# Kernel tuning notes

Hardware: AMD Instinct MI355X
Metric: run time of the kernel (lower is better)

## Reference

```python
import jax, jax.numpy as jnp
import numpy as np

N_HEAD = 16
SCALE = True
NEG = 10000.0


def setup_inputs() -> dict:
    key = jax.random.key(0)
    ks = jax.random.split(key, 5)
    B, S, D = 4, 1024, 1024
    x = jax.random.normal(ks[0], (B, S, D), dtype=jnp.float32)
    # GPT-2 Conv1D weights: W has shape [in, out], init ~N(0, 0.02)
    w_attn = jax.random.normal(ks[1], (D, 3 * D), dtype=jnp.float32) * 0.02
    b_attn = jnp.zeros((3 * D,), dtype=jnp.float32)
    w_proj = jax.random.normal(ks[2], (D, D), dtype=jnp.float32) * 0.02
    b_proj = jnp.zeros((D,), dtype=jnp.float32)
    return {"x": x, "w_attn": w_attn, "b_attn": b_attn,
            "w_proj": w_proj, "b_proj": b_proj}


def reference(x, w_attn, b_attn, w_proj, b_proj):
    B, S, D = x.shape
    H = N_HEAD
    hd = D // H
    # c_attn: Conv1D == x @ W + b
    qkv = jnp.einsum('bsd,de->bse', x, w_attn) + b_attn
    q, k, v = jnp.split(qkv, 3, axis=-1)
    # split heads -> [B, H, S, hd]
    q = q.reshape(B, S, H, hd).transpose(0, 2, 1, 3)
    k = k.reshape(B, S, H, hd).transpose(0, 2, 1, 3)
    v = v.reshape(B, S, H, hd).transpose(0, 2, 1, 3)
    # scores [B, H, S, S]
    w = jnp.einsum('bhqd,bhkd->bhqk', q, k)
    if SCALE:
        w = w / jnp.sqrt(jnp.float32(hd))
    # multiplicative causal mask: w*b - 10000*(1-b)
    bmask = jnp.tril(jnp.ones((S, S), dtype=w.dtype))[None, None]
    w = w * bmask - NEG * (1.0 - bmask)
    w = jax.nn.softmax(w, axis=-1)
    # attn_pdrop = 0 -> dropout is identity
    a = jnp.einsum('bhqk,bhkd->bhqd', w, v)
    # merge heads
    a = a.transpose(0, 2, 1, 3).reshape(B, S, D)
    # c_proj; resid_pdrop = 0
    out = jnp.einsum('bsd,de->bse', a, w_proj) + b_proj
    return out
```

## Files before the change

kernel.cpp:

```cpp
#include <hip/hip_runtime.h>
#include <hip/hip_bf16.h>


typedef __bf16 bf16x8 __attribute__((ext_vector_type(8)));
typedef float f32x4 __attribute__((ext_vector_type(4)));

__device__ __forceinline__ void load_lds16(const void* g, void* l) {
  __builtin_amdgcn_global_load_lds(
      (const __attribute__((address_space(1))) void*)g,
      (__attribute__((address_space(3))) void*)l, 16, 0, 0);
}

__global__ __launch_bounds__(256) void f32_to_bf16(
    const float* __restrict__ in, __bf16* __restrict__ out, int n) {
  int i = (blockIdx.x * 256 + threadIdx.x) * 4;
  if (i + 3 < n) {
    float4 v = *(const float4*)(in + i);
    out[i + 0] = (__bf16)v.x;
    out[i + 1] = (__bf16)v.y;
    out[i + 2] = (__bf16)v.z;
    out[i + 3] = (__bf16)v.w;
  }
}

__global__ __launch_bounds__(256) void transpose_f32_bf16(
    const float* __restrict__ W, __bf16* __restrict__ WT, int K, int N) {
  __shared__ __bf16 tile[32][33];
  int n0 = blockIdx.x * 32, k0 = blockIdx.y * 32;
  int tx = threadIdx.x, ty = threadIdx.y;
#pragma unroll
  for (int j = 0; j < 32; j += 8)
    tile[ty + j][tx] = (__bf16)W[(size_t)(k0 + ty + j) * N + n0 + tx];
  __syncthreads();
#pragma unroll
  for (int j = 0; j < 32; j += 8)
    WT[(size_t)(n0 + ty + j) * K + k0 + tx] = tile[tx][ty + j];
}

__global__ __launch_bounds__(256) void pack_kv(
    const __bf16* __restrict__ qkv, __bf16* __restrict__ Kp,
    __bf16* __restrict__ VT) {
  const int tid = threadIdx.x;
  const int lane = tid & 63, wave = tid >> 6;
  const int bh = blockIdx.x >> 4;
  const int kb = (blockIdx.x & 15) * 64;
  const int b = bh >> 4, h = bh & 15;

  const __bf16* srcv =
      qkv + ((size_t)b * 1024 + kb + lane) * 3072 + 2048 + h * 64 + wave * 16;
  bf16x8 v0 = *(const bf16x8*)srcv;
  bf16x8 v1 = *(const bf16x8*)(srcv + 8);
  __bf16* dstv = VT + ((size_t)bh * 64 + wave * 16) * 1024 + kb + lane;
#pragma unroll
  for (int i = 0; i < 8; ++i) {
    dstv[(size_t)i * 1024] = v0[i];
    dstv[(size_t)(i + 8) * 1024] = v1[i];
  }

#pragma unroll
  for (int p = 0; p < 2; ++p) {
    const int idx = p * 256 + tid;
    const int key = kb + (idx >> 3);
    const int c = (idx & 7) * 8;
    *(bf16x8*)(Kp + (size_t)bh * 65536 + (size_t)key * 64 + c) =
        *(const bf16x8*)(qkv + ((size_t)b * 1024 + key) * 3072 + 1024 + h * 64 + c);
  }
}

template <typename OutT>
__global__ __launch_bounds__(256) void gemm_bt_bias(
    const __bf16* __restrict__ A, const __bf16* __restrict__ BT,
    const float* __restrict__ bias, OutT* __restrict__ C, int M, int N, int K) {
  __shared__ __bf16 sA[128 * 32];
  __shared__ __bf16 sB[128 * 32];

  const int tid = threadIdx.x;
  const int lane = tid & 63;
  const int wave = tid >> 6;
  const int waveM = wave >> 1, waveN = wave & 1;
  const int quad = lane >> 4;
  const int l16 = lane & 15;
  const int rowBase = blockIdx.y * 128;
  const int colBase = blockIdx.x * 128;

  const int rIn = lane >> 2;
  const int sIn = lane & 3;
  const int gc = sIn ^ (rIn & 3) ^ ((rIn >> 2) & 3);
  const int readSlot = quad ^ (l16 & 3) ^ ((l16 >> 2) & 3);

  f32x4 acc[4][4] = {};

  for (int k0 = 0; k0 < K; k0 += 32) {
    __syncthreads();
#pragma unroll
    for (int j = 0; j < 2; ++j) {
      const int rb = wave * 32 + j * 16;
      load_lds16(&A[(size_t)(rowBase + rb + rIn) * K + k0 + gc * 8], &sA[rb * 32]);
      load_lds16(&BT[(size_t)(colBase + rb + rIn) * K + k0 + gc * 8], &sB[rb * 32]);
    }
    __syncthreads();

    bf16x8 af[4], bfr[4];
#pragma unroll
    for (int mt = 0; mt < 4; ++mt)
      af[mt] = *(const bf16x8*)(&sA[(waveM * 64 + mt * 16 + l16) * 32 + readSlot * 8]);
#pragma unroll
    for (int nt = 0; nt < 4; ++nt)
      bfr[nt] = *(const bf16x8*)(&sB[(waveN * 64 + nt * 16 + l16) * 32 + readSlot * 8]);
#pragma unroll
    for (int mt = 0; mt < 4; ++mt)
#pragma unroll
      for (int nt = 0; nt < 4; ++nt)
        acc[mt][nt] = __builtin_amdgcn_mfma_f32_16x16x32_bf16(
            af[mt], bfr[nt], acc[mt][nt], 0, 0, 0);
  }

#pragma unroll
  for (int mt = 0; mt < 4; ++mt) {
    int row = rowBase + waveM * 64 + mt * 16 + quad * 4;
#pragma unroll
    for (int nt = 0; nt < 4; ++nt) {
      int col = colBase + waveN * 64 + nt * 16 + l16;
      float bv = bias[col];
#pragma unroll
      for (int r = 0; r < 4; ++r)
        C[(size_t)(row + r) * N + col] = (OutT)(acc[mt][nt][r] + bv);
    }
  }
}

__global__ __launch_bounds__(256) void attn_mfma(
    const __bf16* __restrict__ qkv, const __bf16* __restrict__ Kp,
    const __bf16* __restrict__ VT, __bf16* __restrict__ Aout) {
  __shared__ __bf16 sK[128 * 64];
  __shared__ __bf16 sV[64 * 128];
  __shared__ __bf16 sP[4 * 16 * 128];

  const int tid = threadIdx.x;
  const int lane = tid & 63;
  const int wave = tid >> 6;
  const int quad = lane >> 4;
  const int l16 = lane & 15;
  const int swq = l16 & 7;

  const int bh = blockIdx.x >> 3;
  const int pr = blockIdx.x & 7;
  const int b = bh >> 4, h = bh & 15;
  const int qbA = pr * 64, qbB = (15 - pr) * 64;
  const int ktA_max = pr >> 1, ktB_max = (15 - pr) >> 1;

  const size_t rowS = 3072;
  const __bf16* Qb = qkv + (size_t)b * 1024 * rowS + h * 64;
  const __bf16* Kb = Kp + (size_t)bh * 65536;
  const __bf16* VTb = VT + (size_t)bh * 64 * 1024;

  bf16x8 qA0A, qA1A, qA0B, qA1B;
  {
    const __bf16* qr = Qb + (size_t)(qbA + wave * 16 + l16) * rowS + quad * 8;
    qA0A = *(const bf16x8*)qr;
    qA1A = *(const bf16x8*)(qr + 32);
    qr = Qb + (size_t)(qbB + wave * 16 + l16) * rowS + quad * 8;
    qA0B = *(const bf16x8*)qr;
    qA1B = *(const bf16x8*)(qr + 32);
  }

  f32x4 OA[4] = {}, OB[4] = {};
  float psA[4] = {0.f, 0.f, 0.f, 0.f}, psB[4] = {0.f, 0.f, 0.f, 0.f};
  __bf16* pw = sP + wave * 2048;

  for (int kt = 0; kt <= ktB_max; ++kt) {
    const int kb = kt * 128;
    __syncthreads();

#pragma unroll
    for (int i = 0; i < 4; ++i) {
      const int rb = wave * 32 + i * 8;
      load_lds16(Kb + (size_t)(kb + rb + (lane >> 3)) * 64 +
                     (((lane & 7) ^ ((lane >> 3) & 7)) << 3),
                 &sK[rb * 64]);
    }
#pragma unroll
    for (int i = 0; i < 4; ++i) {
      const int db = wave * 16 + i * 4;
      const int d = db + (lane >> 4);
      load_lds16(VTb + (size_t)d * 1024 + kb + (((lane & 15) ^ (d & 7)) << 3),
                 &sV[db * 128]);
    }
    __syncthreads();

    {
      float sc[8][4];
#pragma unroll
      for (int n = 0; n < 8; ++n) {
        const int key = n * 16 + l16;
        bf16x8 kB0 = *(const bf16x8*)(&sK[key * 64 + ((quad ^ swq) << 3)]);
        bf16x8 kB1 = *(const bf16x8*)(&sK[key * 64 + (((quad + 4) ^ swq) << 3)]);
        f32x4 c = {};
        c = __builtin_amdgcn_mfma_f32_16x16x32_bf16(qA0B, kB0, c, 0, 0, 0);
        c = __builtin_amdgcn_mfma_f32_16x16x32_bf16(qA1B, kB1, c, 0, 0, 0);
#pragma unroll
        for (int r = 0; r < 4; ++r) sc[n][r] = c[r] * 0.125f;
      }
      if (kt == ktB_max) {
#pragma unroll
        for (int n = 0; n < 8; ++n) {
          const int kg = kb + n * 16 + l16;
#pragma unroll
          for (int r = 0; r < 4; ++r)
            if (kg > qbB + wave * 16 + quad * 4 + r) sc[n][r] = -1.0e30f;
        }
      }
#pragma unroll
      for (int n = 0; n < 8; ++n)
#pragma unroll
        for (int r = 0; r < 4; ++r) {
          float p = __expf(fminf(sc[n][r], 60.0f));
          sc[n][r] = p;
          psB[r] += p;
        }
      {
        const int kb8 = l16 >> 3, lo = l16 & 7;
#pragma unroll
        for (int n = 0; n < 8; ++n) {
          const int chunk = n * 2 + kb8;
#pragma unroll
          for (int r = 0; r < 4; ++r) {
            const int q = quad * 4 + r;
            pw[q * 128 + ((chunk ^ (q & 7)) << 3) + lo] = (__bf16)sc[n][r];
          }
        }
      }
#pragma unroll
      for (int cc = 0; cc < 4; ++cc) {
        bf16x8 pA = *(const bf16x8*)(&pw[l16 * 128 + (((cc * 4 + quad) ^ swq) << 3)]);
#pragma unroll
        for (int nt = 0; nt < 4; ++nt) {
          bf16x8 vB = *(const bf16x8*)(&sV[(nt * 16 + l16) * 128 +
                                           (((cc * 4 + quad) ^ swq) << 3)]);
          OB[nt] = __builtin_amdgcn_mfma_f32_16x16x32_bf16(pA, vB, OB[nt], 0, 0, 0);
        }
      }
    }

    if (kt <= ktA_max) {
      float sc[8][4];
#pragma unroll
      for (int n = 0; n < 8; ++n) {
        const int key = n * 16 + l16;
        bf16x8 kB0 = *(const bf16x8*)(&sK[key * 64 + ((quad ^ swq) << 3)]);
        bf16x8 kB1 = *(const bf16x8*)(&sK[key * 64 + (((quad + 4) ^ swq) << 3)]);
        f32x4 c = {};
        c = __builtin_amdgcn_mfma_f32_16x16x32_bf16(qA0A, kB0, c, 0, 0, 0);
        c = __builtin_amdgcn_mfma_f32_16x16x32_bf16(qA1A, kB1, c, 0, 0, 0);
#pragma unroll
        for (int r = 0; r < 4; ++r) sc[n][r] = c[r] * 0.125f;
      }
      if (kt == ktA_max) {
#pragma unroll
        for (int n = 0; n < 8; ++n) {
          const int kg = kb + n * 16 + l16;
#pragma unroll
          for (int r = 0; r < 4; ++r)
            if (kg > qbA + wave * 16 + quad * 4 + r) sc[n][r] = -1.0e30f;
        }
      }
#pragma unroll
      for (int n = 0; n < 8; ++n)
#pragma unroll
        for (int r = 0; r < 4; ++r) {
          float p = __expf(fminf(sc[n][r], 60.0f));
          sc[n][r] = p;
          psA[r] += p;
        }
      {
        const int kb8 = l16 >> 3, lo = l16 & 7;
#pragma unroll
        for (int n = 0; n < 8; ++n) {
          const int chunk = n * 2 + kb8;
#pragma unroll
          for (int r = 0; r < 4; ++r) {
            const int q = quad * 4 + r;
            pw[q * 128 + ((chunk ^ (q & 7)) << 3) + lo] = (__bf16)sc[n][r];
          }
        }
      }
#pragma unroll
      for (int cc = 0; cc < 4; ++cc) {
        bf16x8 pA = *(const bf16x8*)(&pw[l16 * 128 + (((cc * 4 + quad) ^ swq) << 3)]);
#pragma unroll
        for (int nt = 0; nt < 4; ++nt) {
          bf16x8 vB = *(const bf16x8*)(&sV[(nt * 16 + l16) * 128 +
                                           (((cc * 4 + quad) ^ swq) << 3)]);
          OA[nt] = __builtin_amdgcn_mfma_f32_16x16x32_bf16(pA, vB, OA[nt], 0, 0, 0);
        }
      }
    }
  }

  float invA[4], invB[4];
#pragma unroll
  for (int r = 0; r < 4; ++r) {
    float pa = psA[r], pb = psB[r];
    pa += __shfl_xor(pa, 1); pb += __shfl_xor(pb, 1);
    pa += __shfl_xor(pa, 2); pb += __shfl_xor(pb, 2);
    pa += __shfl_xor(pa, 4); pb += __shfl_xor(pb, 4);
    pa += __shfl_xor(pa, 8); pb += __shfl_xor(pb, 8);
    invA[r] = 1.0f / pa;
    invB[r] = 1.0f / pb;
  }
#pragma unroll
  for (int nt = 0; nt < 4; ++nt) {
#pragma unroll
    for (int r = 0; r < 4; ++r) {
      const int qA = qbA + wave * 16 + quad * 4 + r;
      const int qB = qbB + wave * 16 + quad * 4 + r;
      Aout[((size_t)b * 1024 + qA) * 1024 + h * 64 + nt * 16 + l16] =
          (__bf16)(OA[nt][r] * invA[r]);
      Aout[((size_t)b * 1024 + qB) * 1024 + h * 64 + nt * 16 + l16] =
          (__bf16)(OB[nt][r] * invB[r]);
    }
  }
}

extern "C" void kernel_launch(void* const* d_in, const int* in_sizes, int n_in,
                              void* d_out, int out_size, void* d_ws,
                              size_t ws_size, hipStream_t stream) {
  const float* x      = (const float*)d_in[0];
  const float* w_attn = (const float*)d_in[1];
  const float* b_attn = (const float*)d_in[2];
  const float* w_proj = (const float*)d_in[3];
  const float* b_proj = (const float*)d_in[4];
  float* out = (float*)d_out;

  char* ws = (char*)d_ws;
  __bf16* WT_attn = (__bf16*)(ws);
  __bf16* WT_proj = (__bf16*)(ws + 6291456);
  __bf16* Xb      = (__bf16*)(ws + 8388608);
  __bf16* QKV     = (__bf16*)(ws + 16777216);
  __bf16* Aattn   = (__bf16*)(ws + 41943040);
  __bf16* Kp      = (__bf16*)(ws + 50331648);
  __bf16* VT      = Xb;

  transpose_f32_bf16<<<dim3(96, 32), dim3(32, 8), 0, stream>>>(
      w_attn, WT_attn, 1024, 3072);
  transpose_f32_bf16<<<dim3(32, 32), dim3(32, 8), 0, stream>>>(
      w_proj, WT_proj, 1024, 1024);
  f32_to_bf16<<<4096, 256, 0, stream>>>(x, Xb, 4096 * 1024);
  gemm_bt_bias<__bf16><<<dim3(24, 32), 256, 0, stream>>>(
      Xb, WT_attn, b_attn, QKV, 4096, 3072, 1024);
  pack_kv<<<1024, 256, 0, stream>>>(QKV, Kp, VT);
  attn_mfma<<<512, 256, 0, stream>>>(QKV, Kp, VT, Aattn);
  gemm_bt_bias<float><<<dim3(8, 32), 256, 0, stream>>>(
      Aattn, WT_proj, b_proj, out, 4096, 1024, 1024);
}
```

Baseline: 187.5 us.

## Merge prep kernels, write head-packed Q/K from QKV GEMM, deepen GEMM K-tile

Combines the two weight transposes and the x conversion into one prep launch, with the x cast now vectorized to 16 elements per thread. The QKV GEMM epilogue writes Q and K directly in per-head packed layout and V row-major, so the K-packing pass disappears and only a V transpose remains. The GEMM K-step grows from 32 to 64 with an 8-way XOR swizzle, halving the number of barriers per tile. In exchange the epilogue issues scattered scalar stores, and the larger LDS tiles may reduce occupancy.

```diff
diff --git a/kernel.cpp b/kernel.cpp
--- a/kernel.cpp
+++ b/kernel.cpp
@@ -11,126 +11,162 @@
       (__attribute__((address_space(3))) void*)l, 16, 0, 0);
 }
 
-__global__ __launch_bounds__(256) void f32_to_bf16(
-    const float* __restrict__ in, __bf16* __restrict__ out, int n) {
-  int i = (blockIdx.x * 256 + threadIdx.x) * 4;
-  if (i + 3 < n) {
-    float4 v = *(const float4*)(in + i);
-    out[i + 0] = (__bf16)v.x;
-    out[i + 1] = (__bf16)v.y;
-    out[i + 2] = (__bf16)v.z;
-    out[i + 3] = (__bf16)v.w;
-  }
-}
-
-__global__ __launch_bounds__(256) void transpose_f32_bf16(
-    const float* __restrict__ W, __bf16* __restrict__ WT, int K, int N) {
+__global__ __launch_bounds__(256) void prep(
+    const float* __restrict__ x, const float* __restrict__ w_attn,
+    const float* __restrict__ w_proj, __bf16* __restrict__ Xb,
+    __bf16* __restrict__ WT_attn, __bf16* __restrict__ WT_proj) {
   __shared__ __bf16 tile[32][33];
-  int n0 = blockIdx.x * 32, k0 = blockIdx.y * 32;
-  int tx = threadIdx.x, ty = threadIdx.y;
-#pragma unroll
-  for (int j = 0; j < 32; j += 8)
-    tile[ty + j][tx] = (__bf16)W[(size_t)(k0 + ty + j) * N + n0 + tx];
-  __syncthreads();
-#pragma unroll
-  for (int j = 0; j < 32; j += 8)
-    WT[(size_t)(n0 + ty + j) * K + k0 + tx] = tile[tx][ty + j];
-}
-
-__global__ __launch_bounds__(256) void pack_kv(
-    const __bf16* __restrict__ qkv, __bf16* __restrict__ Kp,
-    __bf16* __restrict__ VT) {
+  const int blk = blockIdx.x;
   const int tid = threadIdx.x;
-  const int lane = tid & 63, wave = tid >> 6;
+  if (blk < 4096) {
+    const float* W;
+    __bf16* WT;
+    int n0, k0, N;
+    if (blk < 3072) {
+      W = w_attn; WT = WT_attn; N = 3072;
+      n0 = (blk % 96) * 32; k0 = (blk / 96) * 32;
+    } else {
+      W = w_proj; WT = WT_proj; N = 1024;
+      const int t = blk - 3072;
+      n0 = (t & 31) * 32; k0 = (t >> 5) * 32;
+    }
+    const int tx = tid & 31, ty = tid >> 5;
+#pragma unroll
+    for (int j = 0; j < 32; j += 8)
+      tile[ty + j][tx] = (__bf16)W[(size_t)(k0 + ty + j) * N + n0 + tx];
+    __syncthreads();
+#pragma unroll
+    for (int j = 0; j < 32; j += 8)
+      WT[(size_t)(n0 + ty + j) * 1024 + k0 + tx] = tile[tx][ty + j];
+  } else {
+    const size_t i = (size_t)(blk - 4096) * 4096 + tid * 16;
+    const float4* xp = (const float4*)(x + i);
+    float4 a = xp[0], b = xp[1], c = xp[2], d = xp[3];
+    bf16x8 o0, o1;
+    o0[0] = (__bf16)a.x; o0[1] = (__bf16)a.y; o0[2] = (__bf16)a.z; o0[3] = (__bf16)a.w;
+    o0[4] = (__bf16)b.x; o0[5] = (__bf16)b.y; o0[6] = (__bf16)b.z; o0[7] = (__bf16)b.w;
+    o1[0] = (__bf16)c.x; o1[1] = (__bf16)c.y; o1[2] = (__bf16)c.z; o1[3] = (__bf16)c.w;
+    o1[4] = (__bf16)d.x; o1[5] = (__bf16)d.y; o1[6] = (__bf16)d.z; o1[7] = (__bf16)d.w;
+    *(bf16x8*)(Xb + i) = o0;
+    *(bf16x8*)(Xb + i + 8) = o1;
+  }
+}
+
+__global__ __launch_bounds__(256) void transpose_v(
+    const __bf16* __restrict__ Vr, __bf16* __restrict__ VT) {
+  const int lane = threadIdx.x & 63, wave = threadIdx.x >> 6;
   const int bh = blockIdx.x >> 4;
   const int kb = (blockIdx.x & 15) * 64;
   const int b = bh >> 4, h = bh & 15;
-
-  const __bf16* srcv =
-      qkv + ((size_t)b * 1024 + kb + lane) * 3072 + 2048 + h * 64 + wave * 16;
-  bf16x8 v0 = *(const bf16x8*)srcv;
-  bf16x8 v1 = *(const bf16x8*)(srcv + 8);
-  __bf16* dstv = VT + ((size_t)bh * 64 + wave * 16) * 1024 + kb + lane;
+  const __bf16* src =
+      Vr + (size_t)(b * 1024 + kb + lane) * 1024 + h * 64 + wave * 16;
+  bf16x8 v0 = *(const bf16x8*)src;
+  bf16x8 v1 = *(const bf16x8*)(src + 8);
+  __bf16* dst = VT + ((size_t)bh * 64 + wave * 16) * 1024 + kb + lane;
 #pragma unroll
   for (int i = 0; i < 8; ++i) {
-    dstv[(size_t)i * 1024] = v0[i];
-    dstv[(size_t)(i + 8) * 1024] = v1[i];
-  }
-
-#pragma unroll
-  for (int p = 0; p < 2; ++p) {
-    const int idx = p * 256 + tid;
-    const int key = kb + (idx >> 3);
-    const int c = (idx & 7) * 8;
-    *(bf16x8*)(Kp + (size_t)bh * 65536 + (size_t)key * 64 + c) =
-        *(const bf16x8*)(qkv + ((size_t)b * 1024 + key) * 3072 + 1024 + h * 64 + c);
-  }
-}
-
-template <typename OutT>
-__global__ __launch_bounds__(256) void gemm_bt_bias(
+    dst[(size_t)i * 1024] = v0[i];
+    dst[(size_t)(i + 8) * 1024] = v1[i];
+  }
+}
+
+#define GEMM_CORE(A_, BT_, K_)                                                   \
+  __shared__ __bf16 sA[128 * 64];                                                \
+  __shared__ __bf16 sB[128 * 64];                                                \
+  const int tid = threadIdx.x;                                                   \
+  const int lane = tid & 63;                                                     \
+  const int wave = tid >> 6;                                                     \
+  const int waveM = wave >> 1, waveN = wave & 1;                                 \
+  const int quad = lane >> 4;                                                    \
+  const int l16 = lane & 15;                                                     \
+  const int rowBase = blockIdx.y * 128;                                          \
+  const int colBase = blockIdx.x * 128;                                          \
+  const int sr = lane >> 3;                                                      \
+  const int ss = lane & 7;                                                       \
+  const int gcs = ss ^ sr;                                                       \
+  const int swl = l16 & 7;                                                       \
+  f32x4 acc[4][4] = {};                                                          \
+  for (int k0 = 0; k0 < K_; k0 += 64) {                                          \
+    __syncthreads();                                                             \
+    _Pragma("unroll") for (int i = 0; i < 4; ++i) {                              \
+      const int rb = wave * 32 + i * 8;                                          \
+      load_lds16(&A_[(size_t)(rowBase + rb + sr) * K_ + k0 + gcs * 8],           \
+                 &sA[rb * 64]);                                                  \
+      load_lds16(&BT_[(size_t)(colBase + rb + sr) * K_ + k0 + gcs * 8],          \
+                 &sB[rb * 64]);                                                  \
+    }                                                                            \
+    __syncthreads();                                                             \
+    bf16x8 af0[4], af1[4], bf0[4], bf1[4];                                       \
+    _Pragma("unroll") for (int mt = 0; mt < 4; ++mt) {                           \
+      const int row = waveM * 64 + mt * 16 + l16;                                \
+      af0[mt] = *(const bf16x8*)(&sA[row * 64 + ((quad ^ swl) << 3)]);           \
+      af1[mt] = *(const bf16x8*)(&sA[row * 64 + (((quad + 4) ^ swl) << 3)]);     \
+    }                                                                            \
+    _Pragma("unroll") for (int nt = 0; nt < 4; ++nt) {                           \
+      const int row = waveN * 64 + nt * 16 + l16;                                \
+      bf0[nt] = *(const bf16x8*)(&sB[row * 64 + ((quad ^ swl) << 3)]);           \
+      bf1[nt] = *(const bf16x8*)(&sB[row * 64 + (((quad + 4) ^ swl) << 3)]);     \
+    }                                                                            \
+    _Pragma("unroll") for (int mt = 0; mt < 4; ++mt)                             \
+    _Pragma("unroll") for (int nt = 0; nt < 4; ++nt) {                           \
+      acc[mt][nt] = __builtin_amdgcn_mfma_f32_16x16x32_bf16(                     \
+          af0[mt], bf0[nt], acc[mt][nt], 0, 0, 0);                               \
+      acc[mt][nt] = __builtin_amdgcn_mfma_f32_16x16x32_bf16(                     \
+          af1[mt], bf1[nt], acc[mt][nt], 0, 0, 0);                               \
+    }                                                                            \
+  }
+
+__global__ __launch_bounds__(256) void gemm_qkv(
     const __bf16* __restrict__ A, const __bf16* __restrict__ BT,
-    const float* __restrict__ bias, OutT* __restrict__ C, int M, int N, int K) {
-  __shared__ __bf16 sA[128 * 32];
-  __shared__ __bf16 sB[128 * 32];
-
-  const int tid = threadIdx.x;
-  const int lane = tid & 63;
-  const int wave = tid >> 6;
-  const int waveM = wave >> 1, waveN = wave & 1;
-  const int quad = lane >> 4;
-  const int l16 = lane & 15;
-  const int rowBase = blockIdx.y * 128;
-  const int colBase = blockIdx.x * 128;
-
-  const int rIn = lane >> 2;
-  const int sIn = lane & 3;
-  const int gc = sIn ^ (rIn & 3) ^ ((rIn >> 2) & 3);
-  const int readSlot = quad ^ (l16 & 3) ^ ((l16 >> 2) & 3);
-
-  f32x4 acc[4][4] = {};
-
-  for (int k0 = 0; k0 < K; k0 += 32) {
-    __syncthreads();
-#pragma unroll
-    for (int j = 0; j < 2; ++j) {
-      const int rb = wave * 32 + j * 16;
-      load_lds16(&A[(size_t)(rowBase + rb + rIn) * K + k0 + gc * 8], &sA[rb * 32]);
-      load_lds16(&BT[(size_t)(colBase + rb + rIn) * K + k0 + gc * 8], &sB[rb * 32]);
-    }
-    __syncthreads();
-
-    bf16x8 af[4], bfr[4];
-#pragma unroll
-    for (int mt = 0; mt < 4; ++mt)
-      af[mt] = *(const bf16x8*)(&sA[(waveM * 64 + mt * 16 + l16) * 32 + readSlot * 8]);
-#pragma unroll
-    for (int nt = 0; nt < 4; ++nt)
-      bfr[nt] = *(const bf16x8*)(&sB[(waveN * 64 + nt * 16 + l16) * 32 + readSlot * 8]);
-#pragma unroll
-    for (int mt = 0; mt < 4; ++mt)
-#pragma unroll
-      for (int nt = 0; nt < 4; ++nt)
-        acc[mt][nt] = __builtin_amdgcn_mfma_f32_16x16x32_bf16(
-            af[mt], bfr[nt], acc[mt][nt], 0, 0, 0);
-  }
-
+    const float* __restrict__ bias, __bf16* __restrict__ Qp,
+    __bf16* __restrict__ Kp, __bf16* __restrict__ Vr) {
+  GEMM_CORE(A, BT, 1024)
+  const int seg = colBase >> 10;
 #pragma unroll
   for (int mt = 0; mt < 4; ++mt) {
-    int row = rowBase + waveM * 64 + mt * 16 + quad * 4;
+    const int row0 = rowBase + waveM * 64 + mt * 16 + quad * 4;
 #pragma unroll
     for (int nt = 0; nt < 4; ++nt) {
-      int col = colBase + waveN * 64 + nt * 16 + l16;
-      float bv = bias[col];
+      const int col = colBase + waveN * 64 + nt * 16 + l16;
+      const float bv = bias[col];
+      const int cc = col & 1023;
+#pragma unroll
+      for (int r = 0; r < 4; ++r) {
+        const int row = row0 + r;
+        const float v = acc[mt][nt][r] + bv;
+        if (seg == 2) {
+          Vr[(size_t)row * 1024 + cc] = (__bf16)v;
+        } else {
+          const int bh = ((row >> 10) << 4) + (cc >> 6);
+          __bf16* dst = (seg == 0) ? Qp : Kp;
+          dst[((size_t)bh << 16) + (size_t)(row & 1023) * 64 + (cc & 63)] =
+              (__bf16)v;
+        }
+      }
+    }
+  }
+}
+
+__global__ __launch_bounds__(256) void gemm_out(
+    const __bf16* __restrict__ A, const __bf16* __restrict__ BT,
+    const float* __restrict__ bias, float* __restrict__ C) {
+  GEMM_CORE(A, BT, 1024)
+#pragma unroll
+  for (int mt = 0; mt < 4; ++mt) {
+    const int row = rowBase + waveM * 64 + mt * 16 + quad * 4;
+#pragma unroll
+    for (int nt = 0; nt < 4; ++nt) {
+      const int col = colBase + waveN * 64 + nt * 16 + l16;
+      const float bv = bias[col];
 #pragma unroll
       for (int r = 0; r < 4; ++r)
-        C[(size_t)(row + r) * N + col] = (OutT)(acc[mt][nt][r] + bv);
+        C[(size_t)(row + r) * 1024 + col] = acc[mt][nt][r] + bv;
     }
   }
 }
 
 __global__ __launch_bounds__(256) void attn_mfma(
-    const __bf16* __restrict__ qkv, const __bf16* __restrict__ Kp,
+    const __bf16* __restrict__ Qp, const __bf16* __restrict__ Kp,
     const __bf16* __restrict__ VT, __bf16* __restrict__ Aout) {
   __shared__ __bf16 sK[128 * 64];
   __shared__ __bf16 sV[64 * 128];
@@ -149,17 +185,16 @@
   const int qbA = pr * 64, qbB = (15 - pr) * 64;
   const int ktA_max = pr >> 1, ktB_max = (15 - pr) >> 1;
 
-  const size_t rowS = 3072;
-  const __bf16* Qb = qkv + (size_t)b * 1024 * rowS + h * 64;
-  const __bf16* Kb = Kp + (size_t)bh * 65536;
+  const __bf16* Qb = Qp + ((size_t)bh << 16);
+  const __bf16* Kb = Kp + ((size_t)bh << 16);
   const __bf16* VTb = VT + (size_t)bh * 64 * 1024;
 
   bf16x8 qA0A, qA1A, qA0B, qA1B;
   {
-    const __bf16* qr = Qb + (size_t)(qbA + wave * 16 + l16) * rowS + quad * 8;
+    const __bf16* qr = Qb + (size_t)(qbA + wave * 16 + l16) * 64 + quad * 8;
     qA0A = *(const bf16x8*)qr;
     qA1A = *(const bf16x8*)(qr + 32);
-    qr = Qb + (size_t)(qbB + wave * 16 + l16) * rowS + quad * 8;
+    qr = Qb + (size_t)(qbB + wave * 16 + l16) * 64 + quad * 8;
     qA0B = *(const bf16x8*)qr;
     qA1B = *(const bf16x8*)(qr + 32);
   }
@@ -336,20 +371,15 @@
   __bf16* WT_attn = (__bf16*)(ws);
   __bf16* WT_proj = (__bf16*)(ws + 6291456);
   __bf16* Xb      = (__bf16*)(ws + 8388608);
-  __bf16* QKV     = (__bf16*)(ws + 16777216);
+  __bf16* Qp      = (__bf16*)(ws + 16777216);
+  __bf16* Kp      = (__bf16*)(ws + 25165824);
+  __bf16* Vr      = (__bf16*)(ws + 33554432);
   __bf16* Aattn   = (__bf16*)(ws + 41943040);
-  __bf16* Kp      = (__bf16*)(ws + 50331648);
   __bf16* VT      = Xb;
 
-  transpose_f32_bf16<<<dim3(96, 32), dim3(32, 8), 0, stream>>>(
-      w_attn, WT_attn, 1024, 3072);
-  transpose_f32_bf16<<<dim3(32, 32), dim3(32, 8), 0, stream>>>(
-      w_proj, WT_proj, 1024, 1024);
-  f32_to_bf16<<<4096, 256, 0, stream>>>(x, Xb, 4096 * 1024);
-  gemm_bt_bias<__bf16><<<dim3(24, 32), 256, 0, stream>>>(
-      Xb, WT_attn, b_attn, QKV, 4096, 3072, 1024);
-  pack_kv<<<1024, 256, 0, stream>>>(QKV, Kp, VT);
-  attn_mfma<<<512, 256, 0, stream>>>(QKV, Kp, VT, Aattn);
-  gemm_bt_bias<float><<<dim3(8, 32), 256, 0, stream>>>(
-      Aattn, WT_proj, b_proj, out, 4096, 1024, 1024);
-}
+  prep<<<5120, 256, 0, stream>>>(x, w_attn, w_proj, Xb, WT_attn, WT_proj);
+  gemm_qkv<<<dim3(24, 32), 256, 0, stream>>>(Xb, WT_attn, b_attn, Qp, Kp, Vr);
+  transpose_v<<<1024, 256, 0, stream>>>(Vr, VT);
+  attn_mfma<<<512, 256, 0, stream>>>(Qp, Kp, VT, Aattn);
+  gemm_out<<<dim3(8, 32), 256, 0, stream>>>(Aattn, WT_proj, b_proj, out);
+}
```

Result: no change. 186.1 us (-0.8%).
